# Kernel optimization log

Measured on AMD Instinct MI355X. Metric: run time of the kernel, lower is better.

The kernel has to match this reference:

```python
import jax, jax.numpy as jnp
import numpy as np

N_NODES = 100000
N_EDGES = 3200000
D_IN = 512
D_OUT = 512


def setup_inputs() -> dict:
    key = jax.random.key(0)
    k1, k2, k3, k4, k5 = jax.random.split(key, 5)
    features = jax.random.normal(k1, (N_NODES, D_IN), dtype=jnp.float32)
    edge_src = jax.random.randint(k2, (N_EDGES,), 0, N_NODES, dtype=jnp.int32)
    edge_dst = jnp.sort(jax.random.randint(k3, (N_EDGES,), 0, N_NODES, dtype=jnp.int32))
    # normalized-adjacency-like positive edge weights
    edge_weight = jax.random.uniform(k4, (N_EDGES,), dtype=jnp.float32)
    # xavier_uniform_ for weight [D_IN, D_OUT]
    limit = float(np.sqrt(6.0 / (D_IN + D_OUT)))
    weight = jax.random.uniform(k5, (D_IN, D_OUT), dtype=jnp.float32,
                                minval=-limit, maxval=limit)
    return {
        "features": features,
        "weight": weight,
        "edge_src": edge_src,
        "edge_dst": edge_dst,
        "edge_weight": edge_weight,
        "times": 3,
    }


def reference(features, weight, edge_src, edge_dst, edge_weight, times):
    n_nodes = features.shape[0]
    # dense feature transform: support = features @ W
    support = features @ weight  # [N, D_OUT]

    def spmm(x):
        # out[dst] += w * x[src]  (one hop of sparse adjacency propagation)
        msgs = x[edge_src] * edge_weight[:, None]  # [E, D_OUT]
        return jax.ops.segment_sum(msgs, edge_dst, num_segments=n_nodes)

    output = spmm(support)
    for _ in range(times - 1):
        output = spmm(output)
    return output
```

## Files before the change

kernel.cpp:

```cpp
#include <hip/hip_runtime.h>

#define N_NODES_C 100000
#define N_EDGES_C 3200000
#define DDIM 512

typedef float v4f __attribute__((ext_vector_type(4)));
typedef unsigned int v4u __attribute__((ext_vector_type(4)));
typedef unsigned short v4h __attribute__((ext_vector_type(4)));
typedef _Float16 v8hf __attribute__((ext_vector_type(8)));

__device__ inline unsigned short f2h(float f) {
    union { _Float16 h; unsigned short u; } v;
    v.h = (_Float16)f;
    return v.u;
}
__device__ inline float h2f(unsigned short s) {
    union { unsigned short u; _Float16 h; } v;
    v.u = s;
    return (float)v.h;
}

__global__ __launch_bounds__(256) void build_rowptr(const int* __restrict__ dst,
                                                    int* __restrict__ rp) {
    int n = blockIdx.x * blockDim.x + threadIdx.x;
    if (n > N_NODES_C) return;
    int lo = 0, hi = N_EDGES_C;
    while (lo < hi) {
        int mid = (lo + hi) >> 1;
        if (dst[mid] < n) lo = mid + 1;
        else hi = mid;
    }
    rp[n] = lo;
}

__global__ __launch_bounds__(256) void gemm_f16(const float* __restrict__ A,
                                                const float* __restrict__ B,
                                                unsigned short* __restrict__ C,
                                                int M) {
    __shared__ unsigned short sA[128][40];
    __shared__ unsigned short sBt[128][40];

    const int tid  = threadIdx.x;
    const int lane = tid & 63;
    const int wave = tid >> 6;
    const int quad = lane >> 4;
    const int l16  = lane & 15;
    const int wr   = (wave >> 1) * 64;
    const int wc   = (wave & 1) * 64;
    const int m0   = blockIdx.x * 128;
    const int n0   = blockIdx.y * 128;

    const int ar = tid >> 3;
    const int ak = (tid & 7) * 4;
    const int bk = tid >> 5;
    const int bc = (tid & 31) * 4;

    v4f acc[4][4] = {};

    for (int k0 = 0; k0 < DDIM; k0 += 32) {
#pragma unroll
        for (int rr = 0; rr < 4; ++rr) {
            const int row = ar + rr * 32;
            const int gm  = m0 + row;
            v4f a4 = {0.f, 0.f, 0.f, 0.f};
            if (gm < M) a4 = *(const v4f*)&A[(size_t)gm * DDIM + k0 + ak];
            v4h h;
            h.x = f2h(a4.x); h.y = f2h(a4.y); h.z = f2h(a4.z); h.w = f2h(a4.w);
            *(v4h*)&sA[row][ak] = h;
        }
#pragma unroll
        for (int kr = 0; kr < 4; ++kr) {
            const int k = bk + kr * 8;
            v4f b4 = *(const v4f*)&B[(size_t)(k0 + k) * DDIM + n0 + bc];
            sBt[bc + 0][k] = f2h(b4.x);
            sBt[bc + 1][k] = f2h(b4.y);
            sBt[bc + 2][k] = f2h(b4.z);
            sBt[bc + 3][k] = f2h(b4.w);
        }
        __syncthreads();

        v8hf af[4], bf[4];
#pragma unroll
        for (int i = 0; i < 4; ++i)
            af[i] = *(const v8hf*)&sA[wr + i * 16 + l16][quad * 8];
#pragma unroll
        for (int j = 0; j < 4; ++j)
            bf[j] = *(const v8hf*)&sBt[wc + j * 16 + l16][quad * 8];
#pragma unroll
        for (int i = 0; i < 4; ++i)
#pragma unroll
            for (int j = 0; j < 4; ++j)
                acc[i][j] = __builtin_amdgcn_mfma_f32_16x16x32_f16(
                    af[i], bf[j], acc[i][j], 0, 0, 0);
        __syncthreads();
    }

#pragma unroll
    for (int i = 0; i < 4; ++i) {
#pragma unroll
        for (int j = 0; j < 4; ++j) {
#pragma unroll
            for (int r = 0; r < 4; ++r) {
                const int rg = m0 + wr + i * 16 + quad * 4 + r;
                const int cg = n0 + wc + j * 16 + l16;
                if (rg < M) C[(size_t)rg * DDIM + cg] = f2h(acc[i][j][r]);
            }
        }
    }
}

__device__ inline void fma8(float* acc, float w, v4u v) {
#pragma unroll
    for (int q = 0; q < 4; ++q) {
        const unsigned int u = v[q];
        acc[2 * q]     = fmaf(w, h2f((unsigned short)(u & 0xffffu)), acc[2 * q]);
        acc[2 * q + 1] = fmaf(w, h2f((unsigned short)(u >> 16)),     acc[2 * q + 1]);
    }
}

template <bool OUT_F32>
__global__ __launch_bounds__(256) void spmm_f16(const v4u* __restrict__ x,
                                                const int* __restrict__ esrc,
                                                const float* __restrict__ ew,
                                                const int* __restrict__ rp,
                                                void* __restrict__ y) {
    const int wave = threadIdx.x >> 6;
    const int lane = threadIdx.x & 63;
    const int n = blockIdx.x * 4 + wave;
    const int s = rp[n];
    const int e = rp[n + 1];

    float a0[8] = {}, a1[8] = {}, a2[8] = {}, a3[8] = {};

    int i = s;
    for (; i + 3 < e; i += 4) {
        const int s0 = esrc[i];
        const int s1 = esrc[i + 1];
        const int s2 = esrc[i + 2];
        const int s3 = esrc[i + 3];
        const float w0 = ew[i];
        const float w1 = ew[i + 1];
        const float w2 = ew[i + 2];
        const float w3 = ew[i + 3];
        v4u v0 = x[(size_t)s0 * 64 + lane];
        v4u v1 = x[(size_t)s1 * 64 + lane];
        v4u v2 = x[(size_t)s2 * 64 + lane];
        v4u v3 = x[(size_t)s3 * 64 + lane];
        fma8(a0, w0, v0);
        fma8(a1, w1, v1);
        fma8(a2, w2, v2);
        fma8(a3, w3, v3);
    }
    for (; i < e; ++i) {
        const int sI = esrc[i];
        const float wI = ew[i];
        v4u vI = x[(size_t)sI * 64 + lane];
        fma8(a0, wI, vI);
    }

    float r[8];
#pragma unroll
    for (int q = 0; q < 8; ++q) r[q] = (a0[q] + a1[q]) + (a2[q] + a3[q]);

    if (OUT_F32) {
        float* yo = (float*)y;
        v4f o0 = {r[0], r[1], r[2], r[3]};
        v4f o1 = {r[4], r[5], r[6], r[7]};
        *(v4f*)&yo[(size_t)n * DDIM + lane * 8] = o0;
        *(v4f*)&yo[(size_t)n * DDIM + lane * 8 + 4] = o1;
    } else {
        v4u o;
        o.x = (unsigned int)f2h(r[0]) | ((unsigned int)f2h(r[1]) << 16);
        o.y = (unsigned int)f2h(r[2]) | ((unsigned int)f2h(r[3]) << 16);
        o.z = (unsigned int)f2h(r[4]) | ((unsigned int)f2h(r[5]) << 16);
        o.w = (unsigned int)f2h(r[6]) | ((unsigned int)f2h(r[7]) << 16);
        ((v4u*)y)[(size_t)n * 64 + lane] = o;
    }
}

extern "C" void kernel_launch(void* const* d_in, const int* in_sizes, int n_in,
                              void* d_out, int out_size, void* d_ws, size_t ws_size,
                              hipStream_t stream) {
    const float* features = (const float*)d_in[0];
    const float* weight   = (const float*)d_in[1];
    const int*   esrc     = (const int*)d_in[2];
    const int*   edst     = (const int*)d_in[3];
    const float* ew       = (const float*)d_in[4];

    float* out = (float*)d_out;
    char*  ws  = (char*)d_ws;

    int* rp = (int*)ws;
    size_t rp_bytes = ((size_t)(N_NODES_C + 1) * sizeof(int) + 511) & ~(size_t)511;
    unsigned short* S = (unsigned short*)(ws + rp_bytes);
    unsigned short* Y = S + (size_t)N_NODES_C * DDIM;

    build_rowptr<<<(N_NODES_C + 256) / 256, 256, 0, stream>>>(edst, rp);

    dim3 ggrid((N_NODES_C + 127) / 128, DDIM / 128);
    gemm_f16<<<ggrid, 256, 0, stream>>>(features, weight, S, N_NODES_C);

    const int sgrid = N_NODES_C / 4;
    spmm_f16<false><<<sgrid, 256, 0, stream>>>((const v4u*)S, esrc, ew, rp, Y);
    spmm_f16<false><<<sgrid, 256, 0, stream>>>((const v4u*)Y, esrc, ew, rp, S);
    spmm_f16<true ><<<sgrid, 256, 0, stream>>>((const v4u*)S, esrc, ew, rp, out);
}
```

Measured before the change: 1.905 ms.

## Pre-convert GEMM operands to fp16 and load tiles via global_load_lds

Adds separate kernels that convert features to fp16 and transpose/convert the weight into fp16, reusing workspace and the output buffer as scratch. The GEMM then streams fp16 tiles directly into LDS with global_load_lds instead of converting in registers and doing scattered transposed LDS stores. This removes per-tile conversion and strided LDS writes but adds an extra full pass over the feature matrix (read fp32, write fp16) and drops the LDS padding, which may cause bank conflicts on fragment reads.

```diff
diff --git a/kernel.cpp b/kernel.cpp
--- a/kernel.cpp
+++ b/kernel.cpp
@@ -6,7 +6,6 @@
 
 typedef float v4f __attribute__((ext_vector_type(4)));
 typedef unsigned int v4u __attribute__((ext_vector_type(4)));
-typedef unsigned short v4h __attribute__((ext_vector_type(4)));
 typedef _Float16 v8hf __attribute__((ext_vector_type(8)));
 
 __device__ inline unsigned short f2h(float f) {
@@ -18,6 +17,13 @@
     union { unsigned short u; _Float16 h; } v;
     v.u = s;
     return (float)v.h;
+}
+
+__device__ __forceinline__ void gload_lds16(const void* g, void* l) {
+    __builtin_amdgcn_global_load_lds(
+        (const __attribute__((address_space(1))) unsigned int*)(void*)(g),
+        (__attribute__((address_space(3))) unsigned int*)(l),
+        16, 0, 0);
 }
 
 __global__ __launch_bounds__(256) void build_rowptr(const int* __restrict__ dst,
@@ -33,12 +39,41 @@
     rp[n] = lo;
 }
 
-__global__ __launch_bounds__(256) void gemm_f16(const float* __restrict__ A,
-                                                const float* __restrict__ B,
-                                                unsigned short* __restrict__ C,
-                                                int M) {
-    __shared__ unsigned short sA[128][40];
-    __shared__ unsigned short sBt[128][40];
+__global__ __launch_bounds__(256) void convert_x(const v4f* __restrict__ X,
+                                                 v4u* __restrict__ Xh) {
+    const size_t i = (size_t)blockIdx.x * 256 + threadIdx.x;
+    const v4f a = X[2 * i];
+    const v4f b = X[2 * i + 1];
+    v4u o;
+    o.x = (unsigned)f2h(a.x) | ((unsigned)f2h(a.y) << 16);
+    o.y = (unsigned)f2h(a.z) | ((unsigned)f2h(a.w) << 16);
+    o.z = (unsigned)f2h(b.x) | ((unsigned)f2h(b.y) << 16);
+    o.w = (unsigned)f2h(b.z) | ((unsigned)f2h(b.w) << 16);
+    Xh[i] = o;
+}
+
+__global__ __launch_bounds__(256) void transpose_b(const float* __restrict__ B,
+                                                   unsigned short* __restrict__ Bt) {
+    __shared__ float t[32][33];
+    const int bk = blockIdx.x * 32;
+    const int bn = blockIdx.y * 32;
+    const int x  = threadIdx.x & 31;
+    const int y0 = threadIdx.x >> 5;
+#pragma unroll
+    for (int r = y0; r < 32; r += 8)
+        t[r][x] = B[(size_t)(bk + r) * DDIM + bn + x];
+    __syncthreads();
+#pragma unroll
+    for (int r = y0; r < 32; r += 8)
+        Bt[(size_t)(bn + r) * DDIM + bk + x] = f2h(t[x][r]);
+}
+
+__global__ __launch_bounds__(256) void gemm3(const unsigned short* __restrict__ Ah,
+                                             const unsigned short* __restrict__ Bt,
+                                             unsigned short* __restrict__ C,
+                                             int M) {
+    __shared__ unsigned short sA[128 * 32];
+    __shared__ unsigned short sB[128 * 32];
 
     const int tid  = threadIdx.x;
     const int lane = tid & 63;
@@ -50,42 +85,35 @@
     const int m0   = blockIdx.x * 128;
     const int n0   = blockIdx.y * 128;
 
-    const int ar = tid >> 3;
-    const int ak = (tid & 7) * 4;
-    const int bk = tid >> 5;
-    const int bc = (tid & 31) * 4;
+    int ar0 = m0 + (tid >> 2);
+    int ar1 = ar0 + 64;
+    if (ar0 >= M) ar0 = 0;
+    if (ar1 >= M) ar1 = 0;
+    const unsigned short* ga0 = Ah + (size_t)ar0 * DDIM + (tid & 3) * 8;
+    const unsigned short* ga1 = Ah + (size_t)ar1 * DDIM + (tid & 3) * 8;
+    const unsigned short* gb0 = Bt + (size_t)(n0 + (tid >> 2)) * DDIM + (tid & 3) * 8;
+    const unsigned short* gb1 = gb0 + (size_t)64 * DDIM;
+    unsigned short* la0 = &sA[wave * 512];
+    unsigned short* la1 = &sA[2048 + wave * 512];
+    unsigned short* lb0 = &sB[wave * 512];
+    unsigned short* lb1 = &sB[2048 + wave * 512];
 
     v4f acc[4][4] = {};
 
     for (int k0 = 0; k0 < DDIM; k0 += 32) {
-#pragma unroll
-        for (int rr = 0; rr < 4; ++rr) {
-            const int row = ar + rr * 32;
-            const int gm  = m0 + row;
-            v4f a4 = {0.f, 0.f, 0.f, 0.f};
-            if (gm < M) a4 = *(const v4f*)&A[(size_t)gm * DDIM + k0 + ak];
-            v4h h;
-            h.x = f2h(a4.x); h.y = f2h(a4.y); h.z = f2h(a4.z); h.w = f2h(a4.w);
-            *(v4h*)&sA[row][ak] = h;
-        }
-#pragma unroll
-        for (int kr = 0; kr < 4; ++kr) {
-            const int k = bk + kr * 8;
-            v4f b4 = *(const v4f*)&B[(size_t)(k0 + k) * DDIM + n0 + bc];
-            sBt[bc + 0][k] = f2h(b4.x);
-            sBt[bc + 1][k] = f2h(b4.y);
-            sBt[bc + 2][k] = f2h(b4.z);
-            sBt[bc + 3][k] = f2h(b4.w);
-        }
+        gload_lds16(ga0 + k0, la0);
+        gload_lds16(ga1 + k0, la1);
+        gload_lds16(gb0 + k0, lb0);
+        gload_lds16(gb1 + k0, lb1);
         __syncthreads();
 
         v8hf af[4], bf[4];
 #pragma unroll
         for (int i = 0; i < 4; ++i)
-            af[i] = *(const v8hf*)&sA[wr + i * 16 + l16][quad * 8];
+            af[i] = *(const v8hf*)&sA[(wr + i * 16 + l16) * 32 + quad * 8];
 #pragma unroll
         for (int j = 0; j < 4; ++j)
-            bf[j] = *(const v8hf*)&sBt[wc + j * 16 + l16][quad * 8];
+            bf[j] = *(const v8hf*)&sB[(wc + j * 16 + l16) * 32 + quad * 8];
 #pragma unroll
         for (int i = 0; i < 4; ++i)
 #pragma unroll
@@ -192,13 +220,20 @@
 
     int* rp = (int*)ws;
     size_t rp_bytes = ((size_t)(N_NODES_C + 1) * sizeof(int) + 511) & ~(size_t)511;
-    unsigned short* S = (unsigned short*)(ws + rp_bytes);
-    unsigned short* Y = S + (size_t)N_NODES_C * DDIM;
+    unsigned short* S  = (unsigned short*)(ws + rp_bytes);
+    unsigned short* Y  = S + (size_t)N_NODES_C * DDIM;
+    unsigned short* Xh = Y;
+    unsigned short* Bt = (unsigned short*)d_out;
 
     build_rowptr<<<(N_NODES_C + 256) / 256, 256, 0, stream>>>(edst, rp);
 
+    convert_x<<<(N_NODES_C * DDIM / 8) / 256, 256, 0, stream>>>(
+        (const v4f*)features, (v4u*)Xh);
+
+    transpose_b<<<dim3(16, 16), 256, 0, stream>>>(weight, Bt);
+
     dim3 ggrid((N_NODES_C + 127) / 128, DDIM / 128);
-    gemm_f16<<<ggrid, 256, 0, stream>>>(features, weight, S, N_NODES_C);
+    gemm3<<<ggrid, 256, 0, stream>>>(Xh, Bt, S, N_NODES_C);
 
     const int sgrid = N_NODES_C / 4;
     spmm_f16<false><<<sgrid, 256, 0, stream>>>((const v4u*)S, esrc, ew, rp, Y);
```

After: 1.767 ms. 7.2% less time.
